# Optimization experiments

Hardware: AMD Instinct MI355X
Metric: run time of the kernel (lower is better)

The kernel has to match this reference:

```python
import jax, jax.numpy as jnp
import numpy as np

NUM_ENTITIES = 100000
NUM_RELATIONS = 500
D = 256            # embedding_dim
T = 4              # num_hash_tables
H = 32             # hash_dim
B = 64             # batch of queries
K = 10
CAND = max(K * 10, int(NUM_ENTITIES * 0.1))  # = 10000


def setup_inputs() -> dict:
    key = jax.random.key(0)
    k0, k1, k2, k3, k4 = jax.random.split(key, 5)
    return {
        "head": jax.random.randint(k0, (B,), 0, NUM_ENTITIES),
        "relation": jax.random.randint(k1, (B,), 0, NUM_RELATIONS),
        "entity_emb": jax.random.normal(k2, (NUM_ENTITIES, D), jnp.float32) * 0.02,
        "relation_emb": jax.random.normal(k3, (NUM_RELATIONS, D), jnp.float32) * 0.02,
        "hash_proj": jax.random.normal(k4, (T, D, H), jnp.float32),
        "k": K,
    }


def reference(head, relation, entity_emb, relation_emb, hash_proj, k):
    # DistMult approximate query path of KnowledgeGraph.query (use_approximate=True).
    h = entity_emb[head]            # [B, D]
    r = relation_emb[relation]      # [B, D]
    target = h * r                  # DistMult target embedding [B, D]

    # LSH hash codes (0/1 floats): projected > 0
    thash = (jnp.einsum('bd,tdh->bth', target, hash_proj) > 0).astype(jnp.float32)      # [B,T,H]
    ahash = (jnp.einsum('nd,tdh->nth', entity_emb, hash_proj) > 0).astype(jnp.float32)  # [N,T,H]

    # Hamming distance over (T,H) bits without materializing [B,N,T,H]:
    # mismatches = sum(a) + sum(b) - 2 * <a,b>  for 0/1 codes
    dot = jnp.einsum('bth,nth->bn', thash, ahash)                                        # [B,N]
    hash_dist = thash.sum((1, 2))[:, None] + ahash.sum((1, 2))[None, :] - 2.0 * dot      # [B,N]

    # top num_candidates with SMALLEST hamming distance
    _, cand_idx = jax.lax.top_k(-hash_dist, CAND)                                        # [B,CAND]

    # DistMult score: (h*r*t).sum(-1) == target . t ; compute dense then gather candidates
    scores_all = jnp.einsum('bd,nd->bn', target, entity_emb)                             # [B,N]
    cand_scores = jnp.take_along_axis(scores_all, cand_idx, axis=1)                      # [B,CAND]

    top_scores, top_local = jax.lax.top_k(cand_scores, k)                                # [B,k]
    top_indices = jnp.take_along_axis(cand_idx, top_local, axis=1)                       # [B,k]
    return top_indices, top_scores
```

## Files before the change

### kernel.cpp

```cpp
#include <hip/hip_runtime.h>
#include <hip/hip_bf16.h>
#include <float.h>

constexpr int NENT  = 100000;
constexpr int DDIM  = 256;
constexpr int BQ    = 64;
constexpr int CANDN = 10000;
constexpr int KTOP  = 10;
constexpr int NSLICE = 16;
constexpr int SLICE  = 6272;
constexpr int HPAD   = 132;

typedef short v8s __attribute__((ext_vector_type(8)));
typedef float v4f __attribute__((ext_vector_type(4)));

__device__ inline void split3(float x, unsigned short& h0, unsigned short& h1,
                              unsigned short& h2) {
    unsigned t0 = __float_as_uint(x) & 0xffff0000u;
    float r1 = x - __uint_as_float(t0);
    unsigned t1 = __float_as_uint(r1) & 0xffff0000u;
    float r2 = r1 - __uint_as_float(t1);
    h0 = (unsigned short)(t0 >> 16);
    h1 = (unsigned short)(t1 >> 16);
    h2 = (unsigned short)(__float_as_uint(r2) >> 16);
}

__device__ inline void split8p(const float* p0, const float* p1,
                               v8s& o0, v8s& o1, v8s& o2) {
    union { v8s v; unsigned short u[8]; } r0, r1, r2;
    float4 f0 = *(const float4*)p0;
    float4 f1 = *(const float4*)(p1);
    float av[8] = {f0.x, f0.y, f0.z, f0.w, f1.x, f1.y, f1.z, f1.w};
    #pragma unroll
    for (int j = 0; j < 8; j++)
        split3(av[j], r0.u[j], r1.u[j], r2.u[j]);
    o0 = r0.v; o1 = r1.v; o2 = r2.v;
}

__device__ inline void stage16(const float* g, float* l) {
    __builtin_amdgcn_global_load_lds(
        (const __attribute__((address_space(1))) void*)g,
        (__attribute__((address_space(3))) void*)l, 16, 0, 0);
}

__global__ __launch_bounds__(256) void k_prep(
    const int* __restrict__ head, const int* __restrict__ rel,
    const float* __restrict__ E, const float* __restrict__ Rm,
    const float* __restrict__ proj,
    float* __restrict__ tgtT, unsigned* __restrict__ thash,
    unsigned short* __restrict__ Whi, unsigned short* __restrict__ Wmid,
    unsigned short* __restrict__ Wlo)
{
    __shared__ float tg[DDIM];
    int blk = blockIdx.x;
    int tid = threadIdx.x;
    if (blk < 128) {
        int c = blk, d = tid;
        float x = proj[((c >> 5)*DDIM + d)*32 + (c & 31)];
        unsigned short h0, h1, h2;
        split3(x, h0, h1, h2);
        Whi [c*DDIM + d] = h0;
        Wmid[c*DDIM + d] = h1;
        Wlo [c*DDIM + d] = h2;
    } else {
        int b = blk - 128;
        int h = head[b], r = rel[b];
        int d = tid;
        float v = E[h*DDIM + d] * Rm[r*DDIM + d];
        tg[d] = v;
        tgtT[d*BQ + b] = v;
        unsigned short h0, h1, h2;
        split3(v, h0, h1, h2);
        int c = 128 + b;
        Whi [c*DDIM + d] = h0;
        Wmid[c*DDIM + d] = h1;
        Wlo [c*DDIM + d] = h2;
        __syncthreads();
        if (tid < 128) {
            int t = tid >> 5, hh = tid & 31;
            float acc = 0.f;
            #pragma unroll 8
            for (int dd = 0; dd < DDIM; dd++)
                acc += tg[dd] * proj[(t*DDIM + dd)*32 + hh];
            unsigned long long m = __ballot(acc > 0.0f);
            int lane = tid & 63, w = tid >> 6;
            if (lane == 0) {
                thash[b*4 + w*2 + 0] = (unsigned)(m & 0xffffffffull);
                thash[b*4 + w*2 + 1] = (unsigned)(m >> 32);
            }
        }
    }
}

constexpr int TILE_E = 128;

__global__ __launch_bounds__(256, 2) void k_gemm(
    const float* __restrict__ E,
    const unsigned short* __restrict__ Whi, const unsigned short* __restrict__ Wmid,
    const unsigned short* __restrict__ Wlo,
    unsigned* __restrict__ ahash, float* __restrict__ scores)
{
    __shared__ __align__(16) float Af[2][TILE_E*32];
    unsigned short* bitsHalf = (unsigned short*)Af;

    int tid = threadIdx.x;
    int l = tid & 63, w = tid >> 6;
    int wm = w >> 1, wn = w & 1;
    int m = l & 15, quad = l >> 4;
    int n0 = blockIdx.x * TILE_E;

    const float* gsrc[4];
    #pragma unroll
    for (int it = 0; it < 4; it++) {
        int U = it*256 + tid;
        int row = U >> 3;
        int us  = (U & 7) ^ (row & 7);
        int n = n0 + row; if (n >= NENT) n = NENT - 1;
        gsrc[it] = E + (size_t)n*DDIM + us*4;
    }

    int offA0[4], offA1[4];
    #pragma unroll
    for (int a = 0; a < 4; a++) {
        int row = wm*64 + a*16 + m;
        offA0[a] = row*32 + (((2*quad)    ) ^ (m & 7))*4;
        offA1[a] = row*32 + (((2*quad) | 1) ^ (m & 7))*4;
    }

    int colOff[6];
    #pragma unroll
    for (int c = 0; c < 6; c++)
        colOff[c] = (wn*96 + c*16 + m)*DDIM + quad*8;

    v4f acc[4][6];
    #pragma unroll
    for (int a = 0; a < 4; a++)
        #pragma unroll
        for (int c = 0; c < 6; c++)
            acc[a][c] = (v4f)0.0f;

    #pragma unroll
    for (int it = 0; it < 4; it++)
        stage16(gsrc[it], &Af[0][(it*256 + w*64)*4]);
    __syncthreads();

    int bb = 0;
    for (int ch = 0; ch < DDIM/32; ch++) {
        if (ch + 1 < DDIM/32) {
            #pragma unroll
            for (int it = 0; it < 4; it++)
                stage16(gsrc[it] + (ch + 1)*32, &Af[bb ^ 1][(it*256 + w*64)*4]);
        }

        v8s a0[4], a1[4], a2[4];
        #pragma unroll
        for (int a = 0; a < 4; a++)
            split8p(&Af[bb][offA0[a]], &Af[bb][offA1[a]], a0[a], a1[a], a2[a]);

        int d0 = ch*32;
        #pragma unroll
        for (int c = 0; c < 6; c++) {
            int co = colOff[c] + d0;
            v8s b0 = *(const v8s*)(Whi  + co);
            v8s b1 = *(const v8s*)(Wmid + co);
            v8s b2 = *(const v8s*)(Wlo  + co);
            #pragma unroll
            for (int a = 0; a < 4; a++) {
                acc[a][c] = __builtin_amdgcn_mfma_f32_16x16x32_bf16(a2[a], b0, acc[a][c], 0, 0, 0);
                acc[a][c] = __builtin_amdgcn_mfma_f32_16x16x32_bf16(a0[a], b2, acc[a][c], 0, 0, 0);
                acc[a][c] = __builtin_amdgcn_mfma_f32_16x16x32_bf16(a1[a], b1, acc[a][c], 0, 0, 0);
                acc[a][c] = __builtin_amdgcn_mfma_f32_16x16x32_bf16(a1[a], b0, acc[a][c], 0, 0, 0);
                acc[a][c] = __builtin_amdgcn_mfma_f32_16x16x32_bf16(a0[a], b1, acc[a][c], 0, 0, 0);
                acc[a][c] = __builtin_amdgcn_mfma_f32_16x16x32_bf16(a0[a], b0, acc[a][c], 0, 0, 0);
            }
        }
        __syncthreads();
        bb ^= 1;
    }

    #pragma unroll
    for (int c = 0; c < 6; c++) {
        int ct = wn*6 + c;
        if (ct < 8) {
            #pragma unroll
            for (int a = 0; a < 4; a++) {
                #pragma unroll
                for (int r = 0; r < 4; r++) {
                    unsigned long long mb = __ballot(acc[a][c][r] > 0.0f);
                    if (m == 0) {
                        int rowl = wm*64 + a*16 + quad*4 + r;
                        bitsHalf[rowl*8 + ct] = (unsigned short)(mb >> (quad*16));
                    }
                }
            }
        } else {
            int b = ct*16 - 128 + m;
            #pragma unroll
            for (int a = 0; a < 4; a++) {
                int nb = n0 + wm*64 + a*16 + quad*4;
                if (nb < NENT)
                    *(float4*)(scores + (size_t)b*NENT + nb) = *(float4*)&acc[a][c];
            }
        }
    }
    __syncthreads();
    if (tid < TILE_E) {
        int n = n0 + tid;
        if (n < NENT)
            *(uint4*)(ahash + (size_t)n*4) = *(const uint4*)&bitsHalf[tid*8];
    }
}

__global__ __launch_bounds__(256) void k_dist(
    const unsigned* __restrict__ ahash, const unsigned* __restrict__ thash,
    unsigned char* __restrict__ dist8, unsigned short* __restrict__ histG)
{
    __shared__ unsigned hist[HPAD][8];
    int s = blockIdx.x, b = blockIdx.y, tid = threadIdx.x;
    int lv = tid & 7;
    for (int i = tid; i < 8*HPAD; i += 256) ((unsigned*)hist)[i] = 0u;
    uint4 tw = *(const uint4*)(thash + b*4);
    __syncthreads();
    int n0 = s*SLICE;
    int n1 = n0 + SLICE; if (n1 > NENT) n1 = NENT;
    unsigned char* drow = dist8 + (size_t)b*NENT;
    for (int n = n0 + tid*4; n < n1; n += 1024) {
        int dv[4];
        #pragma unroll
        for (int i = 0; i < 4; i++) {
            uint4 a = *(const uint4*)(ahash + (size_t)(n+i)*4);
            dv[i] = __popc(a.x^tw.x) + __popc(a.y^tw.y) +
                    __popc(a.z^tw.z) + __popc(a.w^tw.w);
            atomicAdd(&hist[dv[i]][lv], 1u);
        }
        uchar4 o = make_uchar4((unsigned char)dv[0], (unsigned char)dv[1],
                               (unsigned char)dv[2], (unsigned char)dv[3]);
        *(uchar4*)(drow + n) = o;
    }
    __syncthreads();
    unsigned short* hrow = histG + ((size_t)b*NSLICE + s)*HPAD;
    for (int i = tid; i < 129; i += 256) {
        unsigned t = 0;
        #pragma unroll
        for (int v = 0; v < 8; v++) t += hist[i][v];
        hrow[i] = (unsigned short)t;
    }
}

__global__ __launch_bounds__(256) void k_part(
    const unsigned char* __restrict__ dist8, const float* __restrict__ scores,
    const unsigned short* __restrict__ histG,
    const float* __restrict__ tgtT, const float* __restrict__ E,
    float* __restrict__ partS, int* __restrict__ partI)
{
    __shared__ unsigned histT[HPAD];
    __shared__ int dsS, slS, rpS, ncS;
    __shared__ float ls[256];
    __shared__ int   li[256];
    __shared__ float ps[112];
    __shared__ int   pi[112];
    __shared__ int   pcnt;
    __shared__ float TsS; __shared__ int TiS;
    __shared__ int   chosenI[KTOP];
    __shared__ float tgl[DDIM];

    int sl = blockIdx.x, b = blockIdx.y, tid = threadIdx.x;
    const unsigned char* drow = dist8 + (size_t)b*NENT;
    const float* srow = scores + (size_t)b*NENT;

    for (int d = tid; d < 129; d += 256) {
        unsigned sum = 0;
        for (int s = 0; s < NSLICE; s++)
            sum += histG[((size_t)b*NSLICE + s)*HPAD + d];
        histT[d] = sum;
    }
    if (tid == 0) ncS = -1;
    __syncthreads();
    if (tid == 0) {
        unsigned cum = 0; int dss = 128; unsigned R = 1;
        for (int d = 0; d < 129; d++) {
            unsigned c = cum + histT[d];
            if (c >= (unsigned)CANDN) { dss = d; R = (unsigned)CANDN - cum; break; }
            cum = c;
        }
        dsS = dss;
        unsigned acc = 0; slS = NSLICE - 1; rpS = 1;
        for (int s = 0; s < NSLICE; s++) {
            unsigned c = histG[((size_t)b*NSLICE + s)*HPAD + dss];
            if (acc + c >= R) { slS = s; rpS = (int)(R - acc); break; }
            acc += c;
        }
    }
    __syncthreads();
    if (tid < 64) {
        int dss = dsS;
        unsigned Rp = (unsigned)rpS;
        int sBase = slS*SLICE;
        int sEnd = sBase + SLICE; if (sEnd > NENT) sEnd = NENT;
        unsigned cnt = 0;
        for (int base = sBase; base < sEnd; base += 256) {
            unsigned char qa[4];
            #pragma unroll
            for (int s4 = 0; s4 < 4; s4++) {
                int n = base + s4*64 + tid;
                qa[s4] = (n < sEnd) ? drow[n] : (unsigned char)255;
            }
            bool done = false;
            #pragma unroll
            for (int s4 = 0; s4 < 4; s4++) {
                bool eq = (qa[s4] == (unsigned char)dss);
                unsigned long long mm = __ballot(eq);
                unsigned c = __popcll(mm);
                if (cnt + c >= Rp) {
                    unsigned pre = __popcll(mm & ((1ull << tid) - 1ull));
                    if (eq && (cnt + pre + 1u == Rp)) ncS = base + s4*64 + tid;
                    done = true; break;
                }
                cnt += c;
            }
            if (done) break;
        }
    }
    __syncthreads();
    int ds = dsS, nc = ncS;

    int n0 = sl*SLICE;
    int n1 = n0 + SLICE; if (n1 > NENT) n1 = NENT;

    float topS[KTOP]; int topI[KTOP];
    #pragma unroll
    for (int i = 0; i < KTOP; i++) { topS[i] = -FLT_MAX; topI[i] = 0x7fffffff; }

    for (int n = n0 + tid*4; n < n1; n += 1024) {
        uchar4 dv = *(const uchar4*)(drow + n);
        unsigned char da[4] = {dv.x, dv.y, dv.z, dv.w};
        #pragma unroll
        for (int i = 0; i < 4; i++) {
            int d = da[i];
            int nn = n + i;
            if (d < ds || (d == ds && nn <= nc)) {
                float sc = srow[nn];
                if (sc > topS[KTOP-1]) {
                    int p = KTOP - 1;
                    while (p > 0 && topS[p-1] < sc) {
                        topS[p] = topS[p-1]; topI[p] = topI[p-1]; p--;
                    }
                    topS[p] = sc; topI[p] = nn;
                }
            }
        }
    }

    ls[tid] = topS[0]; li[tid] = topI[0];
    if (tid == 0) pcnt = 0;
    if (tid < 112) { ps[tid] = -FLT_MAX; pi[tid] = 0x7fffffff; }
    __syncthreads();

    float mv = topS[0]; int mi = topI[0];
    int rank = 0;
    for (int i = 0; i < 256; i++) {
        float v = ls[i]; int id = li[i];
        rank += (v > mv || (v == mv && id < mi)) ? 1 : 0;
    }
    if (rank == 9 || (rank < 9 && mi == 0x7fffffff)) { TsS = mv; TiS = mi; }
    __syncthreads();
    float ts = TsS; int ti = TiS;

    if (!(ts > mv || (ts == mv && ti < mi))) {
        #pragma unroll
        for (int j = 0; j < KTOP; j++) {
            float sj = topS[j]; int ij = topI[j];
            if (ij == 0x7fffffff) break;
            if (sj > ts || (sj == ts && ij <= ti)) {
                int p = atomicAdd(&pcnt, 1);
                ps[p] = sj; pi[p] = ij;
            } else break;
        }
    }
    __syncthreads();

    if (tid < 112) {
        float s = ps[tid]; int id = pi[tid];
        int r = 0;
        for (int i = 0; i < 112; i++) {
            float v = ps[i]; int iv = pi[i];
            bool beats = (v > s) || (v == s && (iv < id || (iv == id && i < tid)));
            r += beats ? 1 : 0;
        }
        if (r < KTOP) {
            chosenI[r] = id;
            partI[((size_t)b*NSLICE + sl)*KTOP + r] = id;
        }
    }

    for (int d = tid; d < DDIM; d += 256) tgl[d] = tgtT[d*BQ + b];
    __syncthreads();
    if (tid < KTOP) {
        int idx = chosenI[tid];
        float sc = -FLT_MAX;
        if (idx >= 0 && idx < NENT) {
            const float* er = E + (size_t)idx*DDIM;
            float acc = 0.f;
            #pragma unroll 8
            for (int d = 0; d < DDIM; d += 4) {
                float4 v = *(const float4*)(er + d);
                acc += v.x*tgl[d+0];
                acc += v.y*tgl[d+1];
                acc += v.z*tgl[d+2];
                acc += v.w*tgl[d+3];
            }
            sc = acc;
        }
        partS[((size_t)b*NSLICE + sl)*KTOP + tid] = sc;
    }
}

__global__ __launch_bounds__(256) void k_merge(
    const float* __restrict__ partS, const int* __restrict__ partI,
    float* __restrict__ out)
{
    __shared__ float sc2[NSLICE*KTOP];
    __shared__ int   ix2[NSLICE*KTOP];
    int b = blockIdx.x, tid = threadIdx.x;
    if (tid < NSLICE*KTOP) {
        sc2[tid] = partS[(size_t)b*NSLICE*KTOP + tid];
        ix2[tid] = partI[(size_t)b*NSLICE*KTOP + tid];
    }
    __syncthreads();
    if (tid < NSLICE*KTOP) {
        float mv = sc2[tid]; int mi = ix2[tid];
        int rank = 0;
        #pragma unroll 8
        for (int i = 0; i < NSLICE*KTOP; i++) {
            float v = sc2[i]; int id = ix2[i];
            bool beats = (v > mv) ||
                         (v == mv && (id < mi || (id == mi && i < tid)));
            rank += beats ? 1 : 0;
        }
        if (rank < KTOP) {
            out[b*KTOP + rank]           = (float)mi;
            out[BQ*KTOP + b*KTOP + rank] = mv;
        }
    }
}

extern "C" void kernel_launch(void* const* d_in, const int* in_sizes, int n_in,
                              void* d_out, int out_size, void* d_ws, size_t ws_size,
                              hipStream_t stream)
{
    const int*   head = (const int*)d_in[0];
    const int*   rel  = (const int*)d_in[1];
    const float* E    = (const float*)d_in[2];
    const float* Rm   = (const float*)d_in[3];
    const float* proj = (const float*)d_in[4];

    char* ws = (char*)d_ws;
    float*          tgtT   = (float*)(ws);
    unsigned*       thash  = (unsigned*)(ws + 65536);
    unsigned*       ahash  = (unsigned*)(ws + 66560);
    float*          scores = (float*)(ws + 1666560);
    unsigned char*  dist8  = (unsigned char*)(ws + 27266560);
    float*          partS  = (float*)(ws + 33667072);
    int*            partI  = (int*)(ws + 33708032);
    unsigned short* histG  = (unsigned short*)(ws + 33748992);
    unsigned short* Whi    = (unsigned short*)(ws + 34019328);
    unsigned short* Wmid   = (unsigned short*)(ws + 34117632);
    unsigned short* Wlo    = (unsigned short*)(ws + 34215936);
    float*          out    = (float*)d_out;

    hipLaunchKernelGGL(k_prep, dim3(192), dim3(256), 0, stream,
                       head, rel, E, Rm, proj, tgtT, thash, Whi, Wmid, Wlo);
    hipLaunchKernelGGL(k_gemm, dim3((NENT + TILE_E - 1)/TILE_E), dim3(256), 0, stream,
                       E, Whi, Wmid, Wlo, ahash, scores);
    hipLaunchKernelGGL(k_dist, dim3(NSLICE, BQ), dim3(256), 0, stream,
                       ahash, thash, dist8, histG);
    hipLaunchKernelGGL(k_part, dim3(NSLICE, BQ), dim3(256), 0, stream,
                       dist8, scores, histG, tgtT, E, partS, partI);
    hipLaunchKernelGGL(k_merge, dim3(BQ), dim3(256), 0, stream,
                       partS, partI, out);
}
```

Baseline: 318.4 us.

## Fuse distance, partition and merge kernels into one per-query block

Replaces the three tail kernels (distance/histogram, per-slice partial top-k, merge) with a single 1024-thread block per query that keeps the 100000-byte distance row in LDS. This removes the global dist8 and histogram round trips and two kernel launches. Parallelism drops from 1024 blocks to 64 blocks, which leaves most CUs idle on a large GPU. The top-k scan also now runs on only 256 threads over all entities, which lengthens the serial part.

```diff
diff --git a/kernel.cpp b/kernel.cpp
--- a/kernel.cpp
+++ b/kernel.cpp
@@ -7,9 +7,9 @@
 constexpr int BQ    = 64;
 constexpr int CANDN = 10000;
 constexpr int KTOP  = 10;
-constexpr int NSLICE = 16;
-constexpr int SLICE  = 6272;
-constexpr int HPAD   = 132;
+constexpr int KSEL  = 16;
+constexpr int CHUNK = 6272;
+constexpr int HPAD  = 132;
 
 typedef short v8s __attribute__((ext_vector_type(8)));
 typedef float v4f __attribute__((ext_vector_type(4)));
@@ -211,20 +211,36 @@
     }
 }
 
-__global__ __launch_bounds__(256) void k_dist(
+__global__ __launch_bounds__(1024) void k_tail(
     const unsigned* __restrict__ ahash, const unsigned* __restrict__ thash,
-    unsigned char* __restrict__ dist8, unsigned short* __restrict__ histG)
+    const float* __restrict__ scores, const float* __restrict__ tgtT,
+    const float* __restrict__ E, float* __restrict__ out)
 {
+    __shared__ __align__(16) unsigned char distL[NENT];
     __shared__ unsigned hist[HPAD][8];
-    int s = blockIdx.x, b = blockIdx.y, tid = threadIdx.x;
+    __shared__ unsigned histT[HPAD];
+    __shared__ unsigned cw[16];
+    __shared__ int dsS, rS, wS, rpS, ncS;
+    __shared__ float ls[256];
+    __shared__ int   li[256];
+    __shared__ float ps[256];
+    __shared__ int   pi[256];
+    __shared__ int   pcnt;
+    __shared__ float TsS; __shared__ int TiS;
+    __shared__ int   chosen[KSEL];
+    __shared__ float chosenS[KSEL];
+    __shared__ float tgl[DDIM];
+
+    int b = blockIdx.x, tid = threadIdx.x;
+    int lane = tid & 63, wv = tid >> 6;
+    const float* srow = scores + (size_t)b*NENT;
+
+    for (int i = tid; i < 8*HPAD; i += 1024) ((unsigned*)hist)[i] = 0u;
+    uint4 tw = *(const uint4*)(thash + b*4);
+    __syncthreads();
+
     int lv = tid & 7;
-    for (int i = tid; i < 8*HPAD; i += 256) ((unsigned*)hist)[i] = 0u;
-    uint4 tw = *(const uint4*)(thash + b*4);
-    __syncthreads();
-    int n0 = s*SLICE;
-    int n1 = n0 + SLICE; if (n1 > NENT) n1 = NENT;
-    unsigned char* drow = dist8 + (size_t)b*NENT;
-    for (int n = n0 + tid*4; n < n1; n += 1024) {
+    for (int n = tid*4; n < NENT; n += 4096) {
         int dv[4];
         #pragma unroll
         for (int i = 0; i < 4; i++) {
@@ -235,47 +251,19 @@
         }
         uchar4 o = make_uchar4((unsigned char)dv[0], (unsigned char)dv[1],
                                (unsigned char)dv[2], (unsigned char)dv[3]);
-        *(uchar4*)(drow + n) = o;
-    }
-    __syncthreads();
-    unsigned short* hrow = histG + ((size_t)b*NSLICE + s)*HPAD;
-    for (int i = tid; i < 129; i += 256) {
+        *(uchar4*)(distL + n) = o;
+    }
+    __syncthreads();
+
+    for (int i = tid; i < 129; i += 1024) {
         unsigned t = 0;
         #pragma unroll
         for (int v = 0; v < 8; v++) t += hist[i][v];
-        hrow[i] = (unsigned short)t;
-    }
-}
-
-__global__ __launch_bounds__(256) void k_part(
-    const unsigned char* __restrict__ dist8, const float* __restrict__ scores,
-    const unsigned short* __restrict__ histG,
-    const float* __restrict__ tgtT, const float* __restrict__ E,
-    float* __restrict__ partS, int* __restrict__ partI)
-{
-    __shared__ unsigned histT[HPAD];
-    __shared__ int dsS, slS, rpS, ncS;
-    __shared__ float ls[256];
-    __shared__ int   li[256];
-    __shared__ float ps[112];
-    __shared__ int   pi[112];
-    __shared__ int   pcnt;
-    __shared__ float TsS; __shared__ int TiS;
-    __shared__ int   chosenI[KTOP];
-    __shared__ float tgl[DDIM];
-
-    int sl = blockIdx.x, b = blockIdx.y, tid = threadIdx.x;
-    const unsigned char* drow = dist8 + (size_t)b*NENT;
-    const float* srow = scores + (size_t)b*NENT;
-
-    for (int d = tid; d < 129; d += 256) {
-        unsigned sum = 0;
-        for (int s = 0; s < NSLICE; s++)
-            sum += histG[((size_t)b*NSLICE + s)*HPAD + d];
-        histT[d] = sum;
+        histT[i] = t;
     }
     if (tid == 0) ncS = -1;
     __syncthreads();
+
     if (tid == 0) {
         unsigned cum = 0; int dss = 128; unsigned R = 1;
         for (int d = 0; d < 129; d++) {
@@ -283,120 +271,132 @@
             if (c >= (unsigned)CANDN) { dss = d; R = (unsigned)CANDN - cum; break; }
             cum = c;
         }
-        dsS = dss;
-        unsigned acc = 0; slS = NSLICE - 1; rpS = 1;
-        for (int s = 0; s < NSLICE; s++) {
-            unsigned c = histG[((size_t)b*NSLICE + s)*HPAD + dss];
-            if (acc + c >= R) { slS = s; rpS = (int)(R - acc); break; }
+        dsS = dss; rS = (int)R;
+    }
+    __syncthreads();
+    int ds = dsS;
+
+    {
+        int c0 = wv * CHUNK;
+        int c1 = c0 + CHUNK; if (c1 > NENT) c1 = NENT;
+        unsigned cnt = 0;
+        for (int base = c0 + lane*4; base < c1; base += 256) {
+            uchar4 q = *(const uchar4*)(distL + base);
+            cnt += (q.x == (unsigned char)ds) + (q.y == (unsigned char)ds) +
+                   (q.z == (unsigned char)ds) + (q.w == (unsigned char)ds);
+        }
+        #pragma unroll
+        for (int off = 32; off > 0; off >>= 1)
+            cnt += __shfl_down(cnt, off, 64);
+        if (lane == 0) cw[wv] = cnt;
+    }
+    __syncthreads();
+    if (tid == 0) {
+        unsigned R = (unsigned)rS, acc = 0; int w = 15; unsigned rp = R;
+        for (int i = 0; i < 16; i++) {
+            unsigned c = cw[i];
+            if (acc + c >= R) { w = i; rp = R - acc; break; }
             acc += c;
         }
-    }
-    __syncthreads();
-    if (tid < 64) {
-        int dss = dsS;
+        wS = w; rpS = (int)rp;
+    }
+    __syncthreads();
+    if (wv == 0) {
+        int c0 = wS * CHUNK;
+        int c1 = c0 + CHUNK; if (c1 > NENT) c1 = NENT;
         unsigned Rp = (unsigned)rpS;
-        int sBase = slS*SLICE;
-        int sEnd = sBase + SLICE; if (sEnd > NENT) sEnd = NENT;
         unsigned cnt = 0;
-        for (int base = sBase; base < sEnd; base += 256) {
-            unsigned char qa[4];
-            #pragma unroll
-            for (int s4 = 0; s4 < 4; s4++) {
-                int n = base + s4*64 + tid;
-                qa[s4] = (n < sEnd) ? drow[n] : (unsigned char)255;
-            }
-            bool done = false;
-            #pragma unroll
-            for (int s4 = 0; s4 < 4; s4++) {
-                bool eq = (qa[s4] == (unsigned char)dss);
-                unsigned long long mm = __ballot(eq);
-                unsigned c = __popcll(mm);
-                if (cnt + c >= Rp) {
-                    unsigned pre = __popcll(mm & ((1ull << tid) - 1ull));
-                    if (eq && (cnt + pre + 1u == Rp)) ncS = base + s4*64 + tid;
-                    done = true; break;
+        for (int base = c0; base < c1; base += 64) {
+            int n = base + lane;
+            bool eq = (n < c1) && (distL[n] == (unsigned char)ds);
+            unsigned long long mm = __ballot(eq);
+            unsigned c = __popcll(mm);
+            if (cnt + c >= Rp) {
+                unsigned pre = __popcll(mm & ((1ull << lane) - 1ull));
+                if (eq && (cnt + pre + 1u == Rp)) ncS = n;
+                break;
+            }
+            cnt += c;
+        }
+    }
+    __syncthreads();
+    int nc = ncS;
+
+    float topS[KSEL]; int topI[KSEL];
+    #pragma unroll
+    for (int i = 0; i < KSEL; i++) { topS[i] = -FLT_MAX; topI[i] = 0x7fffffff; }
+
+    if (tid < 256) {
+        for (int n = tid*4; n < NENT; n += 1024) {
+            uchar4 q = *(const uchar4*)(distL + n);
+            unsigned char da[4] = {q.x, q.y, q.z, q.w};
+            #pragma unroll
+            for (int i = 0; i < 4; i++) {
+                int d = da[i];
+                int nn = n + i;
+                if (d < ds || (d == ds && nn <= nc)) {
+                    float sc = srow[nn];
+                    if (sc > topS[KSEL-1]) {
+                        int p = KSEL - 1;
+                        while (p > 0 && topS[p-1] < sc) {
+                            topS[p] = topS[p-1]; topI[p] = topI[p-1]; p--;
+                        }
+                        topS[p] = sc; topI[p] = nn;
+                    }
                 }
-                cnt += c;
-            }
-            if (done) break;
-        }
-    }
-    __syncthreads();
-    int ds = dsS, nc = ncS;
-
-    int n0 = sl*SLICE;
-    int n1 = n0 + SLICE; if (n1 > NENT) n1 = NENT;
-
-    float topS[KTOP]; int topI[KTOP];
-    #pragma unroll
-    for (int i = 0; i < KTOP; i++) { topS[i] = -FLT_MAX; topI[i] = 0x7fffffff; }
-
-    for (int n = n0 + tid*4; n < n1; n += 1024) {
-        uchar4 dv = *(const uchar4*)(drow + n);
-        unsigned char da[4] = {dv.x, dv.y, dv.z, dv.w};
-        #pragma unroll
-        for (int i = 0; i < 4; i++) {
-            int d = da[i];
-            int nn = n + i;
-            if (d < ds || (d == ds && nn <= nc)) {
-                float sc = srow[nn];
-                if (sc > topS[KTOP-1]) {
-                    int p = KTOP - 1;
-                    while (p > 0 && topS[p-1] < sc) {
-                        topS[p] = topS[p-1]; topI[p] = topI[p-1]; p--;
-                    }
-                    topS[p] = sc; topI[p] = nn;
-                }
-            }
-        }
-    }
-
-    ls[tid] = topS[0]; li[tid] = topI[0];
+            }
+        }
+    }
+
+    if (tid < 256) { ls[tid] = topS[0]; li[tid] = topI[0];
+                     ps[tid] = -FLT_MAX; pi[tid] = 0x7fffffff; }
     if (tid == 0) pcnt = 0;
-    if (tid < 112) { ps[tid] = -FLT_MAX; pi[tid] = 0x7fffffff; }
     __syncthreads();
 
     float mv = topS[0]; int mi = topI[0];
-    int rank = 0;
-    for (int i = 0; i < 256; i++) {
-        float v = ls[i]; int id = li[i];
-        rank += (v > mv || (v == mv && id < mi)) ? 1 : 0;
-    }
-    if (rank == 9 || (rank < 9 && mi == 0x7fffffff)) { TsS = mv; TiS = mi; }
-    __syncthreads();
-    float ts = TsS; int ti = TiS;
-
-    if (!(ts > mv || (ts == mv && ti < mi))) {
-        #pragma unroll
-        for (int j = 0; j < KTOP; j++) {
-            float sj = topS[j]; int ij = topI[j];
-            if (ij == 0x7fffffff) break;
-            if (sj > ts || (sj == ts && ij <= ti)) {
-                int p = atomicAdd(&pcnt, 1);
-                ps[p] = sj; pi[p] = ij;
-            } else break;
-        }
-    }
-    __syncthreads();
-
-    if (tid < 112) {
+    if (tid < 256) {
+        int rank = 0;
+        for (int i = 0; i < 256; i++) {
+            float v = ls[i]; int id = li[i];
+            rank += (v > mv || (v == mv && id < mi)) ? 1 : 0;
+        }
+        if (rank == KSEL-1 || (rank < KSEL-1 && mi == 0x7fffffff)) {
+            TsS = mv; TiS = mi;
+        }
+    }
+    __syncthreads();
+
+    if (tid < 256) {
+        float ts = TsS; int ti = TiS;
+        if (!(ts > mv || (ts == mv && ti < mi))) {
+            #pragma unroll
+            for (int j = 0; j < KSEL; j++) {
+                float sj = topS[j]; int ij = topI[j];
+                if (ij == 0x7fffffff) break;
+                if (sj > ts || (sj == ts && ij <= ti)) {
+                    int p = atomicAdd(&pcnt, 1);
+                    ps[p] = sj; pi[p] = ij;
+                } else break;
+            }
+        }
+    }
+    __syncthreads();
+
+    if (tid < 256) {
         float s = ps[tid]; int id = pi[tid];
         int r = 0;
-        for (int i = 0; i < 112; i++) {
+        for (int i = 0; i < 256; i++) {
             float v = ps[i]; int iv = pi[i];
             bool beats = (v > s) || (v == s && (iv < id || (iv == id && i < tid)));
             r += beats ? 1 : 0;
         }
-        if (r < KTOP) {
-            chosenI[r] = id;
-            partI[((size_t)b*NSLICE + sl)*KTOP + r] = id;
-        }
-    }
-
-    for (int d = tid; d < DDIM; d += 256) tgl[d] = tgtT[d*BQ + b];
-    __syncthreads();
-    if (tid < KTOP) {
-        int idx = chosenI[tid];
+        if (r < KSEL) chosen[r] = id;
+    }
+    if (tid < 256) tgl[tid] = tgtT[tid*BQ + b];
+    __syncthreads();
+
+    if (tid < KSEL) {
+        int idx = chosen[tid];
         float sc = -FLT_MAX;
         if (idx >= 0 && idx < NENT) {
             const float* er = E + (size_t)idx*DDIM;
@@ -411,35 +411,22 @@
             }
             sc = acc;
         }
-        partS[((size_t)b*NSLICE + sl)*KTOP + tid] = sc;
-    }
-}
-
-__global__ __launch_bounds__(256) void k_merge(
-    const float* __restrict__ partS, const int* __restrict__ partI,
-    float* __restrict__ out)
-{
-    __shared__ float sc2[NSLICE*KTOP];
-    __shared__ int   ix2[NSLICE*KTOP];
-    int b = blockIdx.x, tid = threadIdx.x;
-    if (tid < NSLICE*KTOP) {
-        sc2[tid] = partS[(size_t)b*NSLICE*KTOP + tid];
-        ix2[tid] = partI[(size_t)b*NSLICE*KTOP + tid];
-    }
-    __syncthreads();
-    if (tid < NSLICE*KTOP) {
-        float mv = sc2[tid]; int mi = ix2[tid];
-        int rank = 0;
-        #pragma unroll 8
-        for (int i = 0; i < NSLICE*KTOP; i++) {
-            float v = sc2[i]; int id = ix2[i];
-            bool beats = (v > mv) ||
-                         (v == mv && (id < mi || (id == mi && i < tid)));
-            rank += beats ? 1 : 0;
-        }
-        if (rank < KTOP) {
-            out[b*KTOP + rank]           = (float)mi;
-            out[BQ*KTOP + b*KTOP + rank] = mv;
+        chosenS[tid] = sc;
+    }
+    __syncthreads();
+    if (tid < KSEL) {
+        float mvv = chosenS[tid]; int mii = chosen[tid];
+        int r = 0;
+        #pragma unroll
+        for (int i = 0; i < KSEL; i++) {
+            float v = chosenS[i]; int id = chosen[i];
+            bool beats = (v > mvv) ||
+                         (v == mvv && (id < mii || (id == mii && i < tid)));
+            r += beats ? 1 : 0;
+        }
+        if (r < KTOP) {
+            out[b*KTOP + r]           = (float)mii;
+            out[BQ*KTOP + b*KTOP + r] = mvv;
         }
     }
 }
@@ -459,10 +446,6 @@
     unsigned*       thash  = (unsigned*)(ws + 65536);
     unsigned*       ahash  = (unsigned*)(ws + 66560);
     float*          scores = (float*)(ws + 1666560);
-    unsigned char*  dist8  = (unsigned char*)(ws + 27266560);
-    float*          partS  = (float*)(ws + 33667072);
-    int*            partI  = (int*)(ws + 33708032);
-    unsigned short* histG  = (unsigned short*)(ws + 33748992);
     unsigned short* Whi    = (unsigned short*)(ws + 34019328);
     unsigned short* Wmid   = (unsigned short*)(ws + 34117632);
     unsigned short* Wlo    = (unsigned short*)(ws + 34215936);
@@ -472,10 +455,6 @@
                        head, rel, E, Rm, proj, tgtT, thash, Whi, Wmid, Wlo);
     hipLaunchKernelGGL(k_gemm, dim3((NENT + TILE_E - 1)/TILE_E), dim3(256), 0, stream,
                        E, Whi, Wmid, Wlo, ahash, scores);
-    hipLaunchKernelGGL(k_dist, dim3(NSLICE, BQ), dim3(256), 0, stream,
-                       ahash, thash, dist8, histG);
-    hipLaunchKernelGGL(k_part, dim3(NSLICE, BQ), dim3(256), 0, stream,
-                       dist8, scores, histG, tgtT, E, partS, partI);
-    hipLaunchKernelGGL(k_merge, dim3(BQ), dim3(256), 0, stream,
-                       partS, partI, out);
-}
+    hipLaunchKernelGGL(k_tail, dim3(BQ), dim3(1024), 0, stream,
+                       ahash, thash, scores, tgtT, E, out);
+}
```

Result: slower. 970.7 us (+204.9%).
